# Performance work log

Hardware: AMD Instinct MI355X
Metric: run time of the kernel (lower is better)

Reference implementation:

```python
import jax, jax.numpy as jnp
import numpy as np

N_NODES = 50000
N_EDGES = 1500000
MEM_DIM = 128
EFEAT_DIM = 128
TEMP_DIM = 100


def setup_inputs() -> dict:
    key = jax.random.key(0)
    ks = jax.random.split(key, 10)
    src = jax.random.randint(ks[0], (N_EDGES,), 0, N_NODES)
    dst = jax.random.randint(ks[1], (N_EDGES,), 0, N_NODES)
    edge_ts = jax.random.uniform(ks[2], (N_EDGES,), dtype=jnp.float32) * 100.0
    edge_feats = jax.random.normal(ks[3], (N_EDGES, EFEAT_DIM), dtype=jnp.float32)
    mem_s = jax.random.normal(ks[4], (N_NODES, MEM_DIM), dtype=jnp.float32)
    last_update_t = jax.random.uniform(ks[5], (N_NODES,), dtype=jnp.float32) * 50.0
    # TimeEncode: deterministic init, w = 1/10**linspace(0,9,dim), bias zeros
    time_w = jnp.asarray(1.0 / 10 ** np.linspace(0, 9, TEMP_DIM), dtype=jnp.float32)
    time_b = jnp.zeros((TEMP_DIM,), dtype=jnp.float32)
    msg_dim = MEM_DIM + MEM_DIM + EFEAT_DIM + TEMP_DIM  # 484
    W_ih = jax.random.normal(ks[6], (3 * MEM_DIM, msg_dim), dtype=jnp.float32) * 0.05
    W_hh = jax.random.normal(ks[7], (3 * MEM_DIM, MEM_DIM), dtype=jnp.float32) * 0.05
    b_ih = jax.random.normal(ks[8], (3 * MEM_DIM,), dtype=jnp.float32) * 0.05
    b_hh = jax.random.normal(ks[9], (3 * MEM_DIM,), dtype=jnp.float32) * 0.05
    return {"src": src, "dst": dst, "edge_ts": edge_ts, "edge_feats": edge_feats,
            "mem_s": mem_s, "last_update_t": last_update_t,
            "time_w": time_w, "time_b": time_b,
            "W_ih": W_ih, "W_hh": W_hh, "b_ih": b_ih, "b_hh": b_hh}


def reference(src, dst, edge_ts, edge_feats, mem_s, last_update_t,
              time_w, time_b, W_ih, W_hh, b_ih, b_hh):
    N, H = mem_s.shape
    E = src.shape[0]
    # --- agg_last: per-dst node, pick the incoming edge with max timestamp ---
    max_ts = jax.ops.segment_max(edge_ts, dst, num_segments=N)  # -inf if no msgs
    is_max = edge_ts == max_ts[dst]
    eidx = jnp.arange(E)
    win = jax.ops.segment_max(jnp.where(is_max, eidx, -1), dst, num_segments=N)
    has_msg = win >= 0  # [N]
    w = jnp.clip(win, 0)  # safe index for empty nodes (masked later)
    # --- msg_fn_cat, computed only for the winning edge per node ---
    src_w = src[w]  # [N]
    delta = edge_ts[w] - last_update_t[src_w]  # [N]
    tenc = jnp.cos(delta[:, None] * time_w[None, :] + time_b[None, :])  # [N,T]
    # winning edge's dst == node itself, so edges.dst['s'] == mem_s
    m_bar = jnp.concatenate([mem_s[src_w], mem_s, edge_feats[w], tenc], axis=1)  # [N,484]
    # --- GRUCell(m_bar, mem_s) ---
    gi = m_bar @ W_ih.T + b_ih  # [N, 3H]
    gh = mem_s @ W_hh.T + b_hh  # [N, 3H]
    i_r, i_z, i_n = jnp.split(gi, 3, axis=1)
    h_r, h_z, h_n = jnp.split(gh, 3, axis=1)
    r = jax.nn.sigmoid(i_r + h_r)
    z = jax.nn.sigmoid(i_z + h_z)
    n = jnp.tanh(i_n + r * h_n)
    h_new = (1.0 - z) * n + z * mem_s
    # only nodes that received messages are updated by update_all
    s_out = jnp.where(has_msg[:, None], h_new, mem_s)
    ts_out = jnp.where(has_msg, max_ts, last_update_t)
    return s_out, ts_out
```

## Files before the change

### kernel.cpp

```cpp
#include <hip/hip_runtime.h>
#include <stdint.h>
#include <math.h>

#define N_NODES 50000
#define N_EDGES 1500000
#define HDIM 128
#define TDIM 100
#define KPAD 512
#define BM 64
#define NT 256

typedef __attribute__((ext_vector_type(8))) short short8v;
typedef __attribute__((ext_vector_type(4))) float f32x4;

__device__ __forceinline__ unsigned short f2bf(float x) {
    unsigned int u = __float_as_uint(x);
    return (unsigned short)((u + 0x7fffu + ((u >> 16) & 1u)) >> 16);
}
__device__ __forceinline__ float sigmoidf_(float x) { return 1.0f / (1.0f + __expf(-x)); }
__device__ __forceinline__ float tanhf_(float x) { return 2.0f / (1.0f + __expf(-2.0f * x)) - 1.0f; }

__global__ void init_keys_kernel(unsigned long long* __restrict__ keys) {
    int i = blockIdx.x * 256 + threadIdx.x;
    if (i < N_NODES) keys[i] = 0ULL;
}

__global__ void scan_edges_kernel(const int* __restrict__ dst,
                                  const float* __restrict__ edge_ts,
                                  unsigned long long* __restrict__ keys) {
    int e = blockIdx.x * 256 + threadIdx.x;
    if (e < N_EDGES) {
        unsigned tsb = __float_as_uint(edge_ts[e]);
        int d = dst[e];
        unsigned cur_hi = ((const unsigned*)keys)[2 * d + 1];
        if (tsb >= cur_hi) {
            unsigned long long key =
                ((unsigned long long)tsb << 32) | (unsigned int)(e + 1);
            atomicMax(&keys[d], key);
        }
    }
}

__global__ void convert_w_kernel(const float* __restrict__ Wih, const float* __restrict__ Whh,
                                 unsigned short* __restrict__ wbF1, unsigned short* __restrict__ wbF2) {
    int t = blockIdx.x * 256 + threadIdx.x;
    if (t < 24576) {
        int b = t >> 10, kt = (t >> 6) & 15, l = t & 63;
        int g3 = b >> 3, nq = (b >> 1) & 3, nf = b & 1;
        int srow = g3 * 128 + nq * 32 + nf * 16 + (l & 15);
        int scol = kt * 32 + (l >> 4) * 8;
        unsigned short v[8];
        #pragma unroll
        for (int j = 0; j < 8; ++j)
            v[j] = (scol + j < 484) ? f2bf(Wih[srow * 484 + scol + j]) : (unsigned short)0;
        uint4 pk;
        pk.x = (unsigned)v[0] | ((unsigned)v[1] << 16);
        pk.y = (unsigned)v[2] | ((unsigned)v[3] << 16);
        pk.z = (unsigned)v[4] | ((unsigned)v[5] << 16);
        pk.w = (unsigned)v[6] | ((unsigned)v[7] << 16);
        *(uint4*)&wbF1[(size_t)t * 8] = pk;
    } else if (t < 24576 + 6144) {
        int t2 = t - 24576;
        int b = t2 >> 8, kt = (t2 >> 6) & 3, l = t2 & 63;
        int g3 = b >> 3, nq = (b >> 1) & 3, nf = b & 1;
        int srow = g3 * 128 + nq * 32 + nf * 16 + (l & 15);
        int scol = kt * 32 + (l >> 4) * 8;
        unsigned short v[8];
        #pragma unroll
        for (int j = 0; j < 8; ++j) v[j] = f2bf(Whh[srow * 128 + scol + j]);
        uint4 pk;
        pk.x = (unsigned)v[0] | ((unsigned)v[1] << 16);
        pk.y = (unsigned)v[2] | ((unsigned)v[3] << 16);
        pk.z = (unsigned)v[4] | ((unsigned)v[5] << 16);
        pk.w = (unsigned)v[6] | ((unsigned)v[7] << 16);
        *(uint4*)&wbF2[(size_t)t2 * 8] = pk;
    }
}

__global__ __launch_bounds__(NT, 2)
void gru_mfma_kernel(const int* __restrict__ src,
                     const float* __restrict__ edge_ts,
                     const float* __restrict__ ef,
                     const float* __restrict__ mem,
                     const float* __restrict__ lut,
                     const float* __restrict__ tw,
                     const float* __restrict__ tb,
                     const float* __restrict__ bih,
                     const float* __restrict__ bhh,
                     const unsigned short* __restrict__ wbF1,
                     const unsigned short* __restrict__ wbF2,
                     const unsigned long long* __restrict__ keys,
                     float* __restrict__ out) {
    __shared__ unsigned short Alds[BM * KPAD];
    const int tid = threadIdx.x;
    const int base = blockIdx.x * BM;

    {
        const int i = tid >> 2, l4 = tid & 3;
        const int n = base + i;
        if (n < N_NODES) {
            unsigned long long key = keys[n];
            const int has = (key != 0ULL);
            const int e = has ? (int)((unsigned)key - 1u) : 0;
            const int s = src[e];
            const float tv = edge_ts[e];
            const float d = tv - lut[s];
            if (l4 == 0) out[(size_t)N_NODES * HDIM + n] = has ? tv : lut[n];
            const int swi = i & 7;
            unsigned short* Arow = &Alds[i * KPAD];
            #pragma unroll
            for (int p = 0; p < 16; ++p) {
                const int gk = p * 4 + l4, k0 = gk * 8;
                float f[8];
                if (k0 < 384) {
                    const float* sp = (k0 < 128) ? mem + (size_t)s * HDIM + k0
                                    : (k0 < 256) ? mem + (size_t)n * HDIM + (k0 - 128)
                                                 : ef + (size_t)e * HDIM + (k0 - 256);
                    float4 v0 = *(const float4*)sp;
                    float4 v1 = *(const float4*)(sp + 4);
                    f[0]=v0.x; f[1]=v0.y; f[2]=v0.z; f[3]=v0.w;
                    f[4]=v1.x; f[5]=v1.y; f[6]=v1.z; f[7]=v1.w;
                } else {
                    #pragma unroll
                    for (int j2 = 0; j2 < 8; ++j2) {
                        int q = k0 - 384 + j2;
                        f[j2] = (q < TDIM) ? cosf(fmaf(d, tw[q], tb[q])) : 0.f;
                    }
                }
                uint4 pk;
                pk.x = (unsigned)f2bf(f[0]) | ((unsigned)f2bf(f[1]) << 16);
                pk.y = (unsigned)f2bf(f[2]) | ((unsigned)f2bf(f[3]) << 16);
                pk.z = (unsigned)f2bf(f[4]) | ((unsigned)f2bf(f[5]) << 16);
                pk.w = (unsigned)f2bf(f[6]) | ((unsigned)f2bf(f[7]) << 16);
                *(uint4*)&Arow[(size_t)(gk ^ swi) * 8] = pk;
            }
        }
    }
    __syncthreads();

    const int nq = tid >> 6;
    const int l = tid & 63;
    const int lr = l & 15, lh = l >> 4;

    const f32x4 fzero = {0.f, 0.f, 0.f, 0.f};
    f32x4 acc[4][2][4];
    #pragma unroll
    for (int q = 0; q < 4; ++q)
        #pragma unroll
        for (int nf = 0; nf < 2; ++nf)
            #pragma unroll
            for (int mf = 0; mf < 4; ++mf) acc[q][nf][mf] = fzero;

    #pragma unroll 4
    for (int kt = 0; kt < KPAD / 32; ++kt) {
        const int k0 = kt * 32;
        short8v a[4];
        #pragma unroll
        for (int mf = 0; mf < 4; ++mf) {
            const int row = mf * 16 + lr;
            a[mf] = *(const short8v*)&Alds[row * KPAD + ((k0 + lh * 8) ^ ((row & 7) << 3))];
        }
        #pragma unroll
        for (int g3 = 0; g3 < 3; ++g3)
            #pragma unroll
            for (int nf = 0; nf < 2; ++nf) {
                const int bidx = (g3 * 4 + nq) * 2 + nf;
                short8v b = *(const short8v*)&wbF1[((size_t)(bidx * 16 + kt) * 64 + l) * 8];
                #pragma unroll
                for (int mf = 0; mf < 4; ++mf)
                    acc[g3][nf][mf] = __builtin_amdgcn_mfma_f32_16x16x32_bf16(
                        a[mf], b, acc[g3][nf][mf], 0, 0, 0);
            }
    }
    #pragma unroll
    for (int kt = 0; kt < 4; ++kt) {
        const int kA = 128 + kt * 32;
        short8v a[4];
        #pragma unroll
        for (int mf = 0; mf < 4; ++mf) {
            const int row = mf * 16 + lr;
            a[mf] = *(const short8v*)&Alds[row * KPAD + ((kA + lh * 8) ^ ((row & 7) << 3))];
        }
        #pragma unroll
        for (int g3 = 0; g3 < 3; ++g3)
            #pragma unroll
            for (int nf = 0; nf < 2; ++nf) {
                const int bidx = (g3 * 4 + nq) * 2 + nf;
                short8v b = *(const short8v*)&wbF2[((size_t)(bidx * 4 + kt) * 64 + l) * 8];
                const int q = (g3 < 2) ? g3 : 3;
                #pragma unroll
                for (int mf = 0; mf < 4; ++mf)
                    acc[q][nf][mf] = __builtin_amdgcn_mfma_f32_16x16x32_bf16(
                        a[mf], b, acc[q][nf][mf], 0, 0, 0);
            }
    }

    float br[2], bz[2], bin[2], bhn[2];
    #pragma unroll
    for (int nf = 0; nf < 2; ++nf) {
        const int c = nq * 32 + nf * 16 + lr;
        br[nf] = bih[c] + bhh[c];
        bz[nf] = bih[HDIM + c] + bhh[HDIM + c];
        bin[nf] = bih[2 * HDIM + c];
        bhn[nf] = bhh[2 * HDIM + c];
    }
    #pragma unroll
    for (int mf = 0; mf < 4; ++mf)
        #pragma unroll
        for (int ii = 0; ii < 4; ++ii) {
            const int row = mf * 16 + lh * 4 + ii;
            const int node = base + row;
            if (node >= N_NODES) continue;
            const bool has = keys[node] != 0ULL;
            #pragma unroll
            for (int nf = 0; nf < 2; ++nf) {
                const int c = nq * 32 + nf * 16 + lr;
                const float r = sigmoidf_(acc[0][nf][mf][ii] + br[nf]);
                const float z = sigmoidf_(acc[1][nf][mf][ii] + bz[nf]);
                const float ng = tanhf_(acc[2][nf][mf][ii] + bin[nf] +
                                        r * (acc[3][nf][mf][ii] + bhn[nf]));
                const float h = mem[(size_t)node * HDIM + c];
                out[(size_t)node * HDIM + c] = has ? (1.f - z) * ng + z * h : h;
            }
        }
}

extern "C" void kernel_launch(void* const* d_in, const int* in_sizes, int n_in,
                              void* d_out, int out_size, void* d_ws, size_t ws_size,
                              hipStream_t stream) {
    const int* src       = (const int*)d_in[0];
    const int* dst       = (const int*)d_in[1];
    const float* edge_ts = (const float*)d_in[2];
    const float* ef      = (const float*)d_in[3];
    const float* mem     = (const float*)d_in[4];
    const float* lut     = (const float*)d_in[5];
    const float* tw      = (const float*)d_in[6];
    const float* tb      = (const float*)d_in[7];
    const float* Wih     = (const float*)d_in[8];
    const float* Whh     = (const float*)d_in[9];
    const float* bih     = (const float*)d_in[10];
    const float* bhh     = (const float*)d_in[11];
    float* out = (float*)d_out;

    char* ws = (char*)d_ws;
    unsigned long long* keys = (unsigned long long*)ws;
    unsigned short* wbF1 = (unsigned short*)(ws + 524288);
    unsigned short* wbF2 = (unsigned short*)(ws + 917504);

    init_keys_kernel<<<(N_NODES + 255) / 256, 256, 0, stream>>>(keys);
    scan_edges_kernel<<<(N_EDGES + 255) / 256, 256, 0, stream>>>(dst, edge_ts, keys);
    convert_w_kernel<<<(24576 + 6144 + 255) / 256, 256, 0, stream>>>(Wih, Whh, wbF1, wbF2);
    gru_mfma_kernel<<<(N_NODES + BM - 1) / BM, NT, 0, stream>>>(
        src, edge_ts, ef, mem, lut, tw, tb, bih, bhh, wbF1, wbF2, keys, out);
}
```

Baseline: 146.7 us.

## Split gather/staging into separate kernel writing MFMA-fragment layout to global

The fused GRU kernel used to gather the concatenated message rows into a 64KB LDS tile before running MFMAs. It is now split into a staging kernel and a GEMM kernel. The staging kernel gathers, converts to bf16 and writes a global buffer already in MFMA fragment order. The GEMM kernel then reads A fragments straight from global memory with no LDS, which frees LDS and may raise occupancy, but adds a roughly 51MB global round trip and an extra launch.

```diff
diff --git a/kernel.cpp b/kernel.cpp
--- a/kernel.cpp
+++ b/kernel.cpp
@@ -6,9 +6,8 @@
 #define N_EDGES 1500000
 #define HDIM 128
 #define TDIM 100
-#define KPAD 512
 #define BM 64
-#define NT 256
+#define NTILES ((N_NODES + BM - 1) / BM)
 
 typedef __attribute__((ext_vector_type(8))) short short8v;
 typedef __attribute__((ext_vector_type(4))) float f32x4;
@@ -77,70 +76,80 @@
     }
 }
 
-__global__ __launch_bounds__(NT, 2)
-void gru_mfma_kernel(const int* __restrict__ src,
-                     const float* __restrict__ edge_ts,
-                     const float* __restrict__ ef,
-                     const float* __restrict__ mem,
-                     const float* __restrict__ lut,
-                     const float* __restrict__ tw,
-                     const float* __restrict__ tb,
-                     const float* __restrict__ bih,
-                     const float* __restrict__ bhh,
-                     const unsigned short* __restrict__ wbF1,
-                     const unsigned short* __restrict__ wbF2,
-                     const unsigned long long* __restrict__ keys,
-                     float* __restrict__ out) {
-    __shared__ unsigned short Alds[BM * KPAD];
+__global__ __launch_bounds__(256)
+void stage_kernel(const int* __restrict__ src, const float* __restrict__ edge_ts,
+                  const float* __restrict__ ef, const float* __restrict__ mem,
+                  const float* __restrict__ lut, const float* __restrict__ tw,
+                  const float* __restrict__ tb, const unsigned long long* __restrict__ keys,
+                  unsigned short* __restrict__ Abuf, float* __restrict__ out) {
     const int tid = threadIdx.x;
-    const int base = blockIdx.x * BM;
-
-    {
-        const int i = tid >> 2, l4 = tid & 3;
-        const int n = base + i;
-        if (n < N_NODES) {
-            unsigned long long key = keys[n];
-            const int has = (key != 0ULL);
-            const int e = has ? (int)((unsigned)key - 1u) : 0;
-            const int s = src[e];
-            const float tv = edge_ts[e];
-            const float d = tv - lut[s];
-            if (l4 == 0) out[(size_t)N_NODES * HDIM + n] = has ? tv : lut[n];
-            const int swi = i & 7;
-            unsigned short* Arow = &Alds[i * KPAD];
-            #pragma unroll
-            for (int p = 0; p < 16; ++p) {
-                const int gk = p * 4 + l4, k0 = gk * 8;
-                float f[8];
-                if (k0 < 384) {
-                    const float* sp = (k0 < 128) ? mem + (size_t)s * HDIM + k0
-                                    : (k0 < 256) ? mem + (size_t)n * HDIM + (k0 - 128)
-                                                 : ef + (size_t)e * HDIM + (k0 - 256);
-                    float4 v0 = *(const float4*)sp;
-                    float4 v1 = *(const float4*)(sp + 4);
-                    f[0]=v0.x; f[1]=v0.y; f[2]=v0.z; f[3]=v0.w;
-                    f[4]=v1.x; f[5]=v1.y; f[6]=v1.z; f[7]=v1.w;
-                } else {
-                    #pragma unroll
-                    for (int j2 = 0; j2 < 8; ++j2) {
-                        int q = k0 - 384 + j2;
-                        f[j2] = (q < TDIM) ? cosf(fmaf(d, tw[q], tb[q])) : 0.f;
-                    }
-                }
-                uint4 pk;
-                pk.x = (unsigned)f2bf(f[0]) | ((unsigned)f2bf(f[1]) << 16);
-                pk.y = (unsigned)f2bf(f[2]) | ((unsigned)f2bf(f[3]) << 16);
-                pk.z = (unsigned)f2bf(f[4]) | ((unsigned)f2bf(f[5]) << 16);
-                pk.w = (unsigned)f2bf(f[6]) | ((unsigned)f2bf(f[7]) << 16);
-                *(uint4*)&Arow[(size_t)(gk ^ swi) * 8] = pk;
+    const int gi = blockIdx.x * (256 / 4) + (tid >> 2);
+    const int l4 = tid & 3;
+    if (gi >= NTILES * BM) return;
+    const int mtile = gi >> 6, i = gi & 63;
+    const int mf = i >> 4, lr = i & 15;
+    const int lane = l4 * 16 + lr;
+    unsigned short* abase = Abuf + ((size_t)mtile * 4 + mf) * 16 * 64 * 8;
+
+    if (gi >= N_NODES) {
+        uint4 z = {0u, 0u, 0u, 0u};
+        #pragma unroll
+        for (int p = 0; p < 16; ++p)
+            *(uint4*)&abase[((size_t)p * 64 + lane) * 8] = z;
+        return;
+    }
+
+    const int n = gi;
+    unsigned long long key = keys[n];
+    const int has = (key != 0ULL);
+    const int e = has ? (int)((unsigned)key - 1u) : 0;
+    const int s = src[e];
+    const float tv = edge_ts[e];
+    const float d = tv - lut[s];
+    if (l4 == 0) out[(size_t)N_NODES * HDIM + n] = has ? tv : lut[n];
+
+    #pragma unroll
+    for (int p = 0; p < 16; ++p) {
+        const int k0 = p * 32 + l4 * 8;
+        float f[8];
+        if (k0 < 384) {
+            const float* sp = (k0 < 128) ? mem + (size_t)s * HDIM + k0
+                            : (k0 < 256) ? mem + (size_t)n * HDIM + (k0 - 128)
+                                         : ef + (size_t)e * HDIM + (k0 - 256);
+            float4 v0 = *(const float4*)sp;
+            float4 v1 = *(const float4*)(sp + 4);
+            f[0]=v0.x; f[1]=v0.y; f[2]=v0.z; f[3]=v0.w;
+            f[4]=v1.x; f[5]=v1.y; f[6]=v1.z; f[7]=v1.w;
+        } else {
+            #pragma unroll
+            for (int j2 = 0; j2 < 8; ++j2) {
+                int q = k0 - 384 + j2;
+                f[j2] = (q < TDIM) ? cosf(fmaf(d, tw[q], tb[q])) : 0.f;
             }
         }
-    }
-    __syncthreads();
-
-    const int nq = tid >> 6;
-    const int l = tid & 63;
+        uint4 pk;
+        pk.x = (unsigned)f2bf(f[0]) | ((unsigned)f2bf(f[1]) << 16);
+        pk.y = (unsigned)f2bf(f[2]) | ((unsigned)f2bf(f[3]) << 16);
+        pk.z = (unsigned)f2bf(f[4]) | ((unsigned)f2bf(f[5]) << 16);
+        pk.w = (unsigned)f2bf(f[6]) | ((unsigned)f2bf(f[7]) << 16);
+        *(uint4*)&abase[((size_t)p * 64 + lane) * 8] = pk;
+    }
+}
+
+__global__ __launch_bounds__(256, 2)
+void gemm_kernel(const unsigned short* __restrict__ Abuf,
+                 const unsigned short* __restrict__ wbF1,
+                 const unsigned short* __restrict__ wbF2,
+                 const float* __restrict__ bih, const float* __restrict__ bhh,
+                 const float* __restrict__ mem,
+                 const unsigned long long* __restrict__ keys,
+                 float* __restrict__ out) {
+    const int tid = threadIdx.x;
+    const int bid = blockIdx.x;
+    const int base = bid * BM;
+    const int nq = tid >> 6, l = tid & 63;
     const int lr = l & 15, lh = l >> 4;
+    const unsigned short* abase = Abuf + (size_t)bid * 4 * 16 * 64 * 8;
 
     const f32x4 fzero = {0.f, 0.f, 0.f, 0.f};
     f32x4 acc[4][2][4];
@@ -152,14 +161,11 @@
             for (int mf = 0; mf < 4; ++mf) acc[q][nf][mf] = fzero;
 
     #pragma unroll 4
-    for (int kt = 0; kt < KPAD / 32; ++kt) {
-        const int k0 = kt * 32;
+    for (int kt = 0; kt < 16; ++kt) {
         short8v a[4];
         #pragma unroll
-        for (int mf = 0; mf < 4; ++mf) {
-            const int row = mf * 16 + lr;
-            a[mf] = *(const short8v*)&Alds[row * KPAD + ((k0 + lh * 8) ^ ((row & 7) << 3))];
-        }
+        for (int mf = 0; mf < 4; ++mf)
+            a[mf] = *(const short8v*)&abase[(((size_t)mf * 16 + kt) * 64 + l) * 8];
         #pragma unroll
         for (int g3 = 0; g3 < 3; ++g3)
             #pragma unroll
@@ -173,20 +179,17 @@
             }
     }
     #pragma unroll
-    for (int kt = 0; kt < 4; ++kt) {
-        const int kA = 128 + kt * 32;
+    for (int kt2 = 0; kt2 < 4; ++kt2) {
         short8v a[4];
         #pragma unroll
-        for (int mf = 0; mf < 4; ++mf) {
-            const int row = mf * 16 + lr;
-            a[mf] = *(const short8v*)&Alds[row * KPAD + ((kA + lh * 8) ^ ((row & 7) << 3))];
-        }
+        for (int mf = 0; mf < 4; ++mf)
+            a[mf] = *(const short8v*)&abase[(((size_t)mf * 16 + (4 + kt2)) * 64 + l) * 8];
         #pragma unroll
         for (int g3 = 0; g3 < 3; ++g3)
             #pragma unroll
             for (int nf = 0; nf < 2; ++nf) {
                 const int bidx = (g3 * 4 + nq) * 2 + nf;
-                short8v b = *(const short8v*)&wbF2[((size_t)(bidx * 4 + kt) * 64 + l) * 8];
+                short8v b = *(const short8v*)&wbF2[((size_t)(bidx * 4 + kt2) * 64 + l) * 8];
                 const int q = (g3 < 2) ? g3 : 3;
                 #pragma unroll
                 for (int mf = 0; mf < 4; ++mf)
@@ -246,10 +249,13 @@
     unsigned long long* keys = (unsigned long long*)ws;
     unsigned short* wbF1 = (unsigned short*)(ws + 524288);
     unsigned short* wbF2 = (unsigned short*)(ws + 917504);
+    unsigned short* Abuf = (unsigned short*)(ws + 2097152);
 
     init_keys_kernel<<<(N_NODES + 255) / 256, 256, 0, stream>>>(keys);
     scan_edges_kernel<<<(N_EDGES + 255) / 256, 256, 0, stream>>>(dst, edge_ts, keys);
     convert_w_kernel<<<(24576 + 6144 + 255) / 256, 256, 0, stream>>>(Wih, Whh, wbF1, wbF2);
-    gru_mfma_kernel<<<(N_NODES + BM - 1) / BM, NT, 0, stream>>>(
-        src, edge_ts, ef, mem, lut, tw, tb, bih, bhh, wbF1, wbF2, keys, out);
-}
+    stage_kernel<<<(NTILES * BM * 4 + 255) / 256, 256, 0, stream>>>(
+        src, edge_ts, ef, mem, lut, tw, tb, keys, Abuf, out);
+    gemm_kernel<<<NTILES, 256, 0, stream>>>(
+        Abuf, wbF1, wbF2, bih, bhh, mem, keys, out);
+}
```

Result: slower. 149.9 us (+2.2%).
